# Optimization experiments

Hardware: AMD Instinct MI355X
Metric: run time of the kernel (lower is better)

The kernel has to match this reference:

```python
import math
import jax, jax.numpy as jnp
import numpy as np

B, C, H, W = 2, 512, 64, 64
NUM_HEADS = 8
NUM_GROUPS = 32
EPS = 1e-05
RESCALE = 1.0


def setup_inputs() -> dict:
    key = jax.random.key(0)
    k1, k2, k3 = jax.random.split(key, 3)
    x = jax.random.normal(k1, (B, C, H, W), dtype=jnp.float32)
    norm_w = jnp.ones((C,), dtype=jnp.float32)
    norm_b = jnp.zeros((C,), dtype=jnp.float32)
    qkv_w = jax.random.normal(k2, (3 * C, C), dtype=jnp.float32) * (1.0 / math.sqrt(C))
    qkv_b = jnp.zeros((3 * C,), dtype=jnp.float32)
    proj_w = jax.random.normal(k3, (C, C), dtype=jnp.float32) * (1.0 / math.sqrt(C))
    proj_b = jnp.zeros((C,), dtype=jnp.float32)
    return {"x": x, "norm_w": norm_w, "norm_b": norm_b,
            "qkv_w": qkv_w, "qkv_b": qkv_b, "proj_w": proj_w, "proj_b": proj_b}


def group_norm(x, gamma, beta, num_groups, eps):
    # x: [b, c, h, w]
    b, c = x.shape[0], x.shape[1]
    xg = x.reshape(b, num_groups, -1)  # [b, G, (c//G)*h*w]
    mean = jnp.mean(xg, axis=-1, keepdims=True)
    var = jnp.var(xg, axis=-1, keepdims=True)
    xg = (xg - mean) * jax.lax.rsqrt(var + eps)
    x = xg.reshape(x.shape)
    return x * gamma[None, :, None, None] + beta[None, :, None, None]


def reference(x, norm_w, norm_b, qkv_w, qkv_b, proj_w, proj_b):
    b, c, h, w = x.shape
    L = h * w
    n_heads = NUM_HEADS
    ch = c // n_heads  # per-head channels

    hid = group_norm(x, norm_w, norm_b, NUM_GROUPS, EPS).reshape(b, c, L)
    # 1x1 conv1d == channel matmul
    qkv = jnp.einsum('oc,bcl->bol', qkv_w, hid) + qkv_b[None, :, None]  # [b, 3c, L]
    qkv = qkv.reshape(b * n_heads, 3 * ch, L)
    q, k, v = qkv[:, :ch], qkv[:, ch:2 * ch], qkv[:, 2 * ch:]

    scale = 1.0 / math.sqrt(math.sqrt(ch))
    weight = jnp.einsum('bct,bcs->bts', q * scale, k * scale)  # [b*H, L, L]
    weight = jax.nn.softmax(weight.astype(jnp.float32), axis=-1).astype(weight.dtype)
    a = jnp.einsum('bts,bcs->bct', weight, v)  # [b*H, ch, L]

    hout = a.reshape(b, c, L)
    hout = jnp.einsum('oc,bcl->bol', proj_w, hout) + proj_b[None, :, None]
    hout = hout.reshape(b, c, h, w)
    return (x + hout) / RESCALE
```

## Files before the change

### kernel.cpp

```cpp
#include <hip/hip_runtime.h>
#include <hip/hip_bf16.h>


typedef __attribute__((ext_vector_type(8))) short bf16x8;
typedef __attribute__((ext_vector_type(4))) float f32x4;

#define LL 4096
#define CC 512

__device__ __forceinline__ ushort f2bf(float f) {
    union { float f; unsigned u; } v; v.f = f;
    unsigned u = v.u;
    u += 0x7fffu + ((u >> 16) & 1u);
    return (ushort)(u >> 16);
}

__device__ __forceinline__ float bfly_max16(float x) {
    int a = __float_as_int(x), b = a;
    asm("v_permlane16_swap_b32 %0, %1" : "+v"(a), "+v"(b));
    return fmaxf(__int_as_float(a), __int_as_float(b));
}
__device__ __forceinline__ float bfly_max32(float x) {
    int a = __float_as_int(x), b = a;
    asm("v_permlane32_swap_b32 %0, %1" : "+v"(a), "+v"(b));
    return fmaxf(__int_as_float(a), __int_as_float(b));
}
__device__ __forceinline__ uint cvt_pk_bf16(float lo, float hi) {
    uint r;
    asm("v_cvt_pk_bf16_f32 %0, %1, %2" : "=v"(r) : "v"(lo), "v"(hi));
    return r;
}

__global__ __launch_bounds__(256) void k_convert(
        const float* __restrict__ qkv_w, const float* __restrict__ proj_w,
        ushort* __restrict__ wq, ushort* __restrict__ wp) {
    const int NQ = 1536 * 512;
    int base = (blockIdx.x * 256 + threadIdx.x) * 4;
    const float* src; ushort* dst; int off;
    if (base < NQ) { src = qkv_w; dst = wq; off = base; }
    else           { src = proj_w; dst = wp; off = base - NQ; }
    float4 v = *reinterpret_cast<const float4*>(src + off);
    ushort4 o;
    o.x = f2bf(v.x); o.y = f2bf(v.y); o.z = f2bf(v.z); o.w = f2bf(v.w);
    *reinterpret_cast<ushort4*>(dst + off) = o;
}

__global__ __launch_bounds__(256) void k_gn_part(
        const float* __restrict__ x, float2* __restrict__ part) {
    int bg = blockIdx.x, sl = blockIdx.y;
    const float4* xg = reinterpret_cast<const float4*>(x + (size_t)bg * 65536) + sl * 2048;
    float s = 0.f, ss = 0.f;
    for (int i = threadIdx.x; i < 2048; i += 256) {
        float4 v = xg[i];
        s  += v.x + v.y + v.z + v.w;
        ss += v.x*v.x + v.y*v.y + v.z*v.z + v.w*v.w;
    }
    #pragma unroll
    for (int m = 32; m; m >>= 1) { s += __shfl_xor(s, m); ss += __shfl_xor(ss, m); }
    __shared__ float red[8];
    int wid = threadIdx.x >> 6;
    if ((threadIdx.x & 63) == 0) { red[wid*2] = s; red[wid*2+1] = ss; }
    __syncthreads();
    if (threadIdx.x == 0) {
        s  = red[0] + red[2] + red[4] + red[6];
        ss = red[1] + red[3] + red[5] + red[7];
        part[bg * 8 + sl] = make_float2(s, ss);
    }
}

__global__ void k_gn_stats(const float2* __restrict__ part, float2* __restrict__ stats) {
    int i = threadIdx.x;
    float s = 0.f, ss = 0.f;
    #pragma unroll
    for (int j = 0; j < 8; ++j) { float2 p = part[i*8 + j]; s += p.x; ss += p.y; }
    float mean = s * (1.f/65536.f);
    float var  = ss * (1.f/65536.f) - mean*mean;
    stats[i] = make_float2(mean, rsqrtf(var + 1e-5f));
}

__global__ __launch_bounds__(256) void k_gn_apply(
        const float* __restrict__ x, const float* __restrict__ gamma,
        const float* __restrict__ beta, const float2* __restrict__ stats,
        ushort* __restrict__ hid) {
    int bg = blockIdx.y;
    int b = bg >> 5, c0 = (bg & 31) * 16;
    int l0 = blockIdx.x * 256;
    float2 st = stats[bg];
    __shared__ __align__(16) ushort tile[16][256];
    int tid = threadIdx.x;
    const float* xg = x + (size_t)(b * CC + c0) * LL;
    #pragma unroll
    for (int sub = 0; sub < 4; ++sub) {
        int r = sub * 4 + (tid >> 6);
        int c4 = (tid & 63) * 4;
        float4 v = *reinterpret_cast<const float4*>(xg + (size_t)r * LL + l0 + c4);
        float ga = gamma[c0 + r] * st.y;
        float be = beta[c0 + r] - st.x * ga;
        tile[r][c4+0] = f2bf(v.x * ga + be);
        tile[r][c4+1] = f2bf(v.y * ga + be);
        tile[r][c4+2] = f2bf(v.z * ga + be);
        tile[r][c4+3] = f2bf(v.w * ga + be);
    }
    __syncthreads();
    union { ushort u[16]; uint4 q[2]; } pk;
    #pragma unroll
    for (int r = 0; r < 16; ++r) pk.u[r] = tile[r][tid];
    ushort* dst = hid + ((size_t)b * LL + l0 + tid) * CC + c0;
    *reinterpret_cast<uint4*>(dst)     = pk.q[0];
    *reinterpret_cast<uint4*>(dst + 8) = pk.q[1];
}

#define QSCALE 0.18033688011112042f
__global__ __launch_bounds__(256) void k_qkv(
        const ushort* __restrict__ wq, const ushort* __restrict__ hid,
        const float* __restrict__ qkv_b,
        ushort* __restrict__ q_ws, ushort* __restrict__ k_ws, ushort* __restrict__ v_ws) {
    int b = blockIdx.z;
    int n0 = blockIdx.x * 128;
    int m0 = blockIdx.y * 128;
    int tid = threadIdx.x;
    int w = tid >> 6, lane = tid & 63, h = lane >> 4, lm = lane & 15;
    int m0w = (w & 1) * 64, n0w = (w >> 1) * 64;
    __shared__ __align__(16) ushort As[128][40];
    __shared__ __align__(16) ushort Bs[128][40];
    f32x4 acc[4][4] = {};
    const ushort* Ag = wq + (size_t)m0 * CC;
    const ushort* Bg = hid + (size_t)(b * LL + n0) * CC;
    for (int k0 = 0; k0 < CC; k0 += 32) {
        __syncthreads();
        #pragma unroll
        for (int i = 0; i < 2; ++i) {
            int flat = tid + i * 256;
            int row = flat >> 2, ch = (flat & 3) * 8;
            *reinterpret_cast<uint4*>(&As[row][ch]) =
                *reinterpret_cast<const uint4*>(Ag + (size_t)row * CC + k0 + ch);
            *reinterpret_cast<uint4*>(&Bs[row][ch]) =
                *reinterpret_cast<const uint4*>(Bg + (size_t)row * CC + k0 + ch);
        }
        __syncthreads();
        bf16x8 af[4], bfr[4];
        #pragma unroll
        for (int mi = 0; mi < 4; ++mi)
            af[mi] = *reinterpret_cast<const bf16x8*>(&As[m0w + mi*16 + lm][h*8]);
        #pragma unroll
        for (int nj = 0; nj < 4; ++nj)
            bfr[nj] = *reinterpret_cast<const bf16x8*>(&Bs[n0w + nj*16 + lm][h*8]);
        #pragma unroll
        for (int mi = 0; mi < 4; ++mi)
            #pragma unroll
            for (int nj = 0; nj < 4; ++nj)
                acc[mi][nj] = __builtin_amdgcn_mfma_f32_16x16x32_bf16(af[mi], bfr[nj], acc[mi][nj], 0, 0, 0);
    }
    #pragma unroll
    for (int mi = 0; mi < 4; ++mi) {
        int o_base = m0 + m0w + mi * 16 + h * 4;
        float4 bias = *reinterpret_cast<const float4*>(qkv_b + o_base);
        int head = o_base / 192;
        int rem  = o_base - head * 192;
        int part = rem >> 6;
        int ch   = rem & 63;
        #pragma unroll
        for (int nj = 0; nj < 4; ++nj) {
            int l = n0 + n0w + nj * 16 + lm;
            float v0 = acc[mi][nj][0] + bias.x;
            float v1 = acc[mi][nj][1] + bias.y;
            float v2 = acc[mi][nj][2] + bias.z;
            float v3 = acc[mi][nj][3] + bias.w;
            if (part == 0) {
                ushort4 pk;
                pk.x = f2bf(v0 * QSCALE); pk.y = f2bf(v1 * QSCALE);
                pk.z = f2bf(v2 * QSCALE); pk.w = f2bf(v3 * QSCALE);
                *reinterpret_cast<ushort4*>(q_ws + ((size_t)(b*8 + head) * LL + l) * 64 + ch) = pk;
            } else if (part == 1) {
                ushort4 pk;
                pk.x = f2bf(v0); pk.y = f2bf(v1); pk.z = f2bf(v2); pk.w = f2bf(v3);
                *reinterpret_cast<ushort4*>(k_ws + ((size_t)(b*8 + head) * LL + l) * 64 + ch) = pk;
            } else {
                ushort* vp = v_ws + ((size_t)(b*8 + head) * 64 + ch) * LL + l;
                vp[0] = f2bf(v0); vp[LL] = f2bf(v1); vp[2*LL] = f2bf(v2); vp[3*LL] = f2bf(v3);
            }
        }
    }
}

__global__ __launch_bounds__(256) void k_attn(
        const ushort* __restrict__ q_ws, const ushort* __restrict__ k_ws,
        const ushort* __restrict__ v_ws, ushort* __restrict__ o_ws) {
    int bh = blockIdx.y;
    int tid = threadIdx.x;
    int w = tid >> 6, lane = tid & 63, h = lane >> 4, lm = lane & 15;
    int t0 = blockIdx.x * 128 + w * 32;

    __shared__ __align__(16) ushort Ks [2][64][72];
    __shared__ __align__(16) ushort Vts[2][64][72];

    bf16x8 bQ[2][2];
    {
        const ushort* qp = q_ws + ((size_t)bh * LL + t0 + lm) * 64 + h * 8;
        bQ[0][0] = *reinterpret_cast<const bf16x8*>(qp);
        bQ[0][1] = *reinterpret_cast<const bf16x8*>(qp + 32);
        bQ[1][0] = *reinterpret_cast<const bf16x8*>(qp + 16 * 64);
        bQ[1][1] = *reinterpret_cast<const bf16x8*>(qp + 16 * 64 + 32);
    }
    bf16x8 aOnes;
    {
        short v = (lm == 0) ? (short)0x3F80 : (short)0;
        #pragma unroll
        for (int j = 0; j < 8; ++j) aOnes[j] = v;
    }

    int srow = lane >> 3, scol = (lane & 7) * 8;
    const ushort* kgp = k_ws + ((size_t)bh * LL + w * 16 + srow) * 64 + scol;
    const ushort* vgp = v_ws + ((size_t)bh * 64 + w * 16 + srow) * LL + scol;
    uint4 kr0, kr1, vr0, vr1;
    auto issue = [&]() {
        kr0 = *reinterpret_cast<const uint4*>(kgp);
        kr1 = *reinterpret_cast<const uint4*>(kgp + 8 * 64);
        vr0 = *reinterpret_cast<const uint4*>(vgp);
        vr1 = *reinterpret_cast<const uint4*>(vgp + 8 * LL);
        kgp += 64 * 64;
        vgp += 64;
    };
    issue();

    float mr[2] = {-1e30f, -1e30f};
    f32x4 accO[2][5] = {};

    for (int t = 0; t < 64; ++t) {
        int p = t & 1;
        {
            int row = w * 16 + srow;
            *reinterpret_cast<uint4*>(&Ks [p][row    ][scol]) = kr0;
            *reinterpret_cast<uint4*>(&Ks [p][row + 8][scol]) = kr1;
            *reinterpret_cast<uint4*>(&Vts[p][row    ][scol]) = vr0;
            *reinterpret_cast<uint4*>(&Vts[p][row + 8][scol]) = vr1;
        }
        if (t < 63) issue();
        __syncthreads();

        f32x4 sf[2][4] = {};
        __builtin_amdgcn_s_setprio(1);
        #pragma unroll
        for (int ss = 0; ss < 4; ++ss)
            #pragma unroll
            for (int kc = 0; kc < 2; ++kc) {
                bf16x8 aK = *reinterpret_cast<const bf16x8*>(&Ks[p][ss*16 + lm][kc*32 + h*8]);
                sf[0][ss] = __builtin_amdgcn_mfma_f32_16x16x32_bf16(aK, bQ[0][kc], sf[0][ss], 0, 0, 0);
                sf[1][ss] = __builtin_amdgcn_mfma_f32_16x16x32_bf16(aK, bQ[1][kc], sf[1][ss], 0, 0, 0);
            }
        __builtin_amdgcn_s_setprio(0);

        #pragma unroll
        for (int qt = 0; qt < 2; ++qt) {
            float a0 = fmaxf(fmaxf(sf[qt][0][0], sf[qt][0][1]), fmaxf(sf[qt][0][2], sf[qt][0][3]));
            float a1 = fmaxf(fmaxf(sf[qt][1][0], sf[qt][1][1]), fmaxf(sf[qt][1][2], sf[qt][1][3]));
            float a2 = fmaxf(fmaxf(sf[qt][2][0], sf[qt][2][1]), fmaxf(sf[qt][2][2], sf[qt][2][3]));
            float a3 = fmaxf(fmaxf(sf[qt][3][0], sf[qt][3][1]), fmaxf(sf[qt][3][2], sf[qt][3][3]));
            float tm = fmaxf(fmaxf(a0, a1), fmaxf(a2, a3));
            tm = bfly_max16(tm);
            tm = bfly_max32(tm);
            if (!__all(tm <= mr[qt] + 8.f)) {
                float mn = fmaxf(mr[qt], tm);
                float corr = __builtin_amdgcn_exp2f(mr[qt] - mn);
                mr[qt] = mn;
                #pragma unroll
                for (int nj = 0; nj < 5; ++nj)
                    #pragma unroll
                    for (int r = 0; r < 4; ++r)
                        accO[qt][nj][r] *= corr;
            }
            #pragma unroll
            for (int ss = 0; ss < 4; ++ss)
                #pragma unroll
                for (int r = 0; r < 4; ++r)
                    sf[qt][ss][r] = __builtin_amdgcn_exp2f(sf[qt][ss][r] - mr[qt]);

            bf16x8 bP[2];
            #pragma unroll
            for (int kc = 0; kc < 2; ++kc) {
                uint a = cvt_pk_bf16(sf[qt][2*kc  ][0], sf[qt][2*kc  ][1]);
                uint b = cvt_pk_bf16(sf[qt][2*kc  ][2], sf[qt][2*kc  ][3]);
                uint c = cvt_pk_bf16(sf[qt][2*kc+1][0], sf[qt][2*kc+1][1]);
                uint d = cvt_pk_bf16(sf[qt][2*kc+1][2], sf[qt][2*kc+1][3]);
                asm("v_permlane32_swap_b32 %0, %1" : "+v"(a), "+v"(c));
                asm("v_permlane32_swap_b32 %0, %1" : "+v"(b), "+v"(d));
                asm("v_permlane16_swap_b32 %0, %1" : "+v"(a), "+v"(c));
                asm("v_permlane16_swap_b32 %0, %1" : "+v"(b), "+v"(d));
                union { uint u[4]; bf16x8 v; } pw;
                pw.u[0] = a; pw.u[1] = b; pw.u[2] = c; pw.u[3] = d;
                bP[kc] = pw.v;
            }

            __builtin_amdgcn_s_setprio(1);
            #pragma unroll
            for (int kc = 0; kc < 2; ++kc) {
                #pragma unroll
                for (int nj = 0; nj < 4; ++nj) {
                    bf16x8 aV = *reinterpret_cast<const bf16x8*>(&Vts[p][nj*16 + lm][kc*32 + h*8]);
                    accO[qt][nj] = __builtin_amdgcn_mfma_f32_16x16x32_bf16(aV, bP[kc], accO[qt][nj], 0, 0, 0);
                }
                accO[qt][4] = __builtin_amdgcn_mfma_f32_16x16x32_bf16(aOnes, bP[kc], accO[qt][4], 0, 0, 0);
            }
            __builtin_amdgcn_s_setprio(0);
        }
    }

    #pragma unroll
    for (int qt = 0; qt < 2; ++qt) {
        float l  = __shfl(accO[qt][4][0], lm);
        float iv = 1.f / l;
        #pragma unroll
        for (int nj = 0; nj < 4; ++nj) {
            ushort4 o4;
            o4.x = f2bf(accO[qt][nj][0] * iv);
            o4.y = f2bf(accO[qt][nj][1] * iv);
            o4.z = f2bf(accO[qt][nj][2] * iv);
            o4.w = f2bf(accO[qt][nj][3] * iv);
            *reinterpret_cast<ushort4*>(
                o_ws + ((size_t)bh * LL + t0 + qt*16 + lm) * 64 + nj*16 + h*4) = o4;
        }
    }
}

__global__ __launch_bounds__(256) void k_proj(
        const ushort* __restrict__ wp, const ushort* __restrict__ o_ws,
        const float* __restrict__ proj_b, const float* __restrict__ x,
        float* __restrict__ out) {
    int b = blockIdx.z;
    int n0 = blockIdx.x * 128;
    int m0 = blockIdx.y * 128;
    int tid = threadIdx.x;
    int w = tid >> 6, lane = tid & 63, h = lane >> 4, lm = lane & 15;
    int m0w = (w & 1) * 64, n0w = (w >> 1) * 64;
    __shared__ __align__(16) ushort As[128][40];
    __shared__ __align__(16) ushort Bs[128][40];
    f32x4 acc[4][4] = {};
    const ushort* Ag = wp + (size_t)m0 * CC;
    for (int k0 = 0; k0 < CC; k0 += 32) {
        const ushort* Bg = o_ws + ((size_t)(b * 8 + (k0 >> 6)) * LL + n0) * 64 + (k0 & 63);
        __syncthreads();
        #pragma unroll
        for (int i = 0; i < 2; ++i) {
            int flat = tid + i * 256;
            int row = flat >> 2, ch = (flat & 3) * 8;
            *reinterpret_cast<uint4*>(&As[row][ch]) =
                *reinterpret_cast<const uint4*>(Ag + (size_t)row * CC + k0 + ch);
            *reinterpret_cast<uint4*>(&Bs[row][ch]) =
                *reinterpret_cast<const uint4*>(Bg + (size_t)row * 64 + ch);
        }
        __syncthreads();
        bf16x8 af[4], bfr[4];
        #pragma unroll
        for (int mi = 0; mi < 4; ++mi)
            af[mi] = *reinterpret_cast<const bf16x8*>(&As[m0w + mi*16 + lm][h*8]);
        #pragma unroll
        for (int nj = 0; nj < 4; ++nj)
            bfr[nj] = *reinterpret_cast<const bf16x8*>(&Bs[n0w + nj*16 + lm][h*8]);
        #pragma unroll
        for (int mi = 0; mi < 4; ++mi)
            #pragma unroll
            for (int nj = 0; nj < 4; ++nj)
                acc[mi][nj] = __builtin_amdgcn_mfma_f32_16x16x32_bf16(af[mi], bfr[nj], acc[mi][nj], 0, 0, 0);
    }
    #pragma unroll
    for (int mi = 0; mi < 4; ++mi) {
        int o = m0 + m0w + mi * 16 + h * 4;
        float4 bias = *reinterpret_cast<const float4*>(proj_b + o);
        #pragma unroll
        for (int nj = 0; nj < 4; ++nj) {
            int l = n0 + n0w + nj * 16 + lm;
            size_t xo = (size_t)(b * CC + o) * LL + l;
            out[xo]          = acc[mi][nj][0] + bias.x + x[xo];
            out[xo +   LL]   = acc[mi][nj][1] + bias.y + x[xo +   LL];
            out[xo + 2*LL]   = acc[mi][nj][2] + bias.z + x[xo + 2*LL];
            out[xo + 3*LL]   = acc[mi][nj][3] + bias.w + x[xo + 3*LL];
        }
    }
}

extern "C" void kernel_launch(void* const* d_in, const int* in_sizes, int n_in,
                              void* d_out, int out_size, void* d_ws, size_t ws_size,
                              hipStream_t stream) {
    const float* x      = (const float*)d_in[0];
    const float* norm_w = (const float*)d_in[1];
    const float* norm_b = (const float*)d_in[2];
    const float* qkv_w  = (const float*)d_in[3];
    const float* qkv_b  = (const float*)d_in[4];
    const float* proj_w = (const float*)d_in[5];
    const float* proj_b = (const float*)d_in[6];
    float* out = (float*)d_out;
    char* ws = (char*)d_ws;

    ushort* wq    = (ushort*)(ws);
    ushort* wp    = (ushort*)(ws + 1572864);
    ushort* hid   = (ushort*)(ws + 2097152);
    ushort* q_ws  = (ushort*)(ws + 10485760);
    ushort* k_ws  = (ushort*)(ws + 18874368);
    ushort* v_ws  = (ushort*)(ws + 27262976);
    ushort* o_ws  = (ushort*)(ws + 35651584);
    float2* part  = (float2*)(ws + 44040192);
    float2* stats = (float2*)(ws + 44044288);

    k_convert<<<dim3(1024), dim3(256), 0, stream>>>(qkv_w, proj_w, wq, wp);
    k_gn_part<<<dim3(64, 8), dim3(256), 0, stream>>>(x, part);
    k_gn_stats<<<dim3(1), dim3(64), 0, stream>>>(part, stats);
    k_gn_apply<<<dim3(16, 64), dim3(256), 0, stream>>>(x, norm_w, norm_b, stats, hid);
    k_qkv<<<dim3(32, 12, 2), dim3(256), 0, stream>>>(wq, hid, qkv_b, q_ws, k_ws, v_ws);
    k_attn<<<dim3(32, 16), dim3(256), 0, stream>>>(q_ws, k_ws, v_ws, o_ws);
    k_proj<<<dim3(32, 4, 2), dim3(256), 0, stream>>>(wp, o_ws, proj_b, x, out);
}
```

Baseline: 174.0 us.

## Split attention KV range across two warp groups and switch to fp16

Every bf16 intermediate and MFMA is switched to fp16. The attention kernel now launches 512 threads, and two groups of four waves each process half of the key/value sequence. The groups merge their partial softmax states (max, sum, accumulator) through shared memory at the end. The ones-vector MFMA that computed the row sum is replaced by explicit lane reductions. The aim is more waves per block and fewer serial KV iterations per wave, paid for with a merge step, more shared memory, fp16 range risk, and removal of the lazy-rescale threshold, so rescaling happens more often.

```diff
diff --git a/kernel.cpp b/kernel.cpp
--- a/kernel.cpp
+++ b/kernel.cpp
@@ -2,17 +2,16 @@
 #include <hip/hip_bf16.h>
 
 
-typedef __attribute__((ext_vector_type(8))) short bf16x8;
+typedef _Float16 f16;
+typedef __attribute__((ext_vector_type(8))) _Float16 f16x8;
 typedef __attribute__((ext_vector_type(4))) float f32x4;
 
 #define LL 4096
 #define CC 512
 
-__device__ __forceinline__ ushort f2bf(float f) {
-    union { float f; unsigned u; } v; v.f = f;
-    unsigned u = v.u;
-    u += 0x7fffu + ((u >> 16) & 1u);
-    return (ushort)(u >> 16);
+__device__ __forceinline__ ushort f2h(float f) {
+    f16 h = (f16)f;
+    return *reinterpret_cast<ushort*>(&h);
 }
 
 __device__ __forceinline__ float bfly_max16(float x) {
@@ -25,10 +24,20 @@
     asm("v_permlane32_swap_b32 %0, %1" : "+v"(a), "+v"(b));
     return fmaxf(__int_as_float(a), __int_as_float(b));
 }
-__device__ __forceinline__ uint cvt_pk_bf16(float lo, float hi) {
-    uint r;
-    asm("v_cvt_pk_bf16_f32 %0, %1, %2" : "=v"(r) : "v"(lo), "v"(hi));
-    return r;
+__device__ __forceinline__ float bfly_add16(float x) {
+    int a = __float_as_int(x), b = a;
+    asm("v_permlane16_swap_b32 %0, %1" : "+v"(a), "+v"(b));
+    return __int_as_float(a) + __int_as_float(b);
+}
+__device__ __forceinline__ float bfly_add32(float x) {
+    int a = __float_as_int(x), b = a;
+    asm("v_permlane32_swap_b32 %0, %1" : "+v"(a), "+v"(b));
+    return __int_as_float(a) + __int_as_float(b);
+}
+__device__ __forceinline__ uint pkh(float lo, float hi) {
+    union { decltype(__builtin_amdgcn_cvt_pkrtz(0.f, 0.f)) h; uint u; } r;
+    r.h = __builtin_amdgcn_cvt_pkrtz(lo, hi);
+    return r.u;
 }
 
 __global__ __launch_bounds__(256) void k_convert(
@@ -41,7 +50,7 @@
     else           { src = proj_w; dst = wp; off = base - NQ; }
     float4 v = *reinterpret_cast<const float4*>(src + off);
     ushort4 o;
-    o.x = f2bf(v.x); o.y = f2bf(v.y); o.z = f2bf(v.z); o.w = f2bf(v.w);
+    o.x = f2h(v.x); o.y = f2h(v.y); o.z = f2h(v.z); o.w = f2h(v.w);
     *reinterpret_cast<ushort4*>(dst + off) = o;
 }
 
@@ -96,10 +105,10 @@
         float4 v = *reinterpret_cast<const float4*>(xg + (size_t)r * LL + l0 + c4);
         float ga = gamma[c0 + r] * st.y;
         float be = beta[c0 + r] - st.x * ga;
-        tile[r][c4+0] = f2bf(v.x * ga + be);
-        tile[r][c4+1] = f2bf(v.y * ga + be);
-        tile[r][c4+2] = f2bf(v.z * ga + be);
-        tile[r][c4+3] = f2bf(v.w * ga + be);
+        tile[r][c4+0] = f2h(v.x * ga + be);
+        tile[r][c4+1] = f2h(v.y * ga + be);
+        tile[r][c4+2] = f2h(v.z * ga + be);
+        tile[r][c4+3] = f2h(v.w * ga + be);
     }
     __syncthreads();
     union { ushort u[16]; uint4 q[2]; } pk;
@@ -138,18 +147,18 @@
                 *reinterpret_cast<const uint4*>(Bg + (size_t)row * CC + k0 + ch);
         }
         __syncthreads();
-        bf16x8 af[4], bfr[4];
+        f16x8 af[4], bfr[4];
         #pragma unroll
         for (int mi = 0; mi < 4; ++mi)
-            af[mi] = *reinterpret_cast<const bf16x8*>(&As[m0w + mi*16 + lm][h*8]);
+            af[mi] = *reinterpret_cast<const f16x8*>(&As[m0w + mi*16 + lm][h*8]);
         #pragma unroll
         for (int nj = 0; nj < 4; ++nj)
-            bfr[nj] = *reinterpret_cast<const bf16x8*>(&Bs[n0w + nj*16 + lm][h*8]);
+            bfr[nj] = *reinterpret_cast<const f16x8*>(&Bs[n0w + nj*16 + lm][h*8]);
         #pragma unroll
         for (int mi = 0; mi < 4; ++mi)
             #pragma unroll
             for (int nj = 0; nj < 4; ++nj)
-                acc[mi][nj] = __builtin_amdgcn_mfma_f32_16x16x32_bf16(af[mi], bfr[nj], acc[mi][nj], 0, 0, 0);
+                acc[mi][nj] = __builtin_amdgcn_mfma_f32_16x16x32_f16(af[mi], bfr[nj], acc[mi][nj], 0, 0, 0);
     }
     #pragma unroll
     for (int mi = 0; mi < 4; ++mi) {
@@ -168,50 +177,47 @@
             float v3 = acc[mi][nj][3] + bias.w;
             if (part == 0) {
                 ushort4 pk;
-                pk.x = f2bf(v0 * QSCALE); pk.y = f2bf(v1 * QSCALE);
-                pk.z = f2bf(v2 * QSCALE); pk.w = f2bf(v3 * QSCALE);
+                pk.x = f2h(v0 * QSCALE); pk.y = f2h(v1 * QSCALE);
+                pk.z = f2h(v2 * QSCALE); pk.w = f2h(v3 * QSCALE);
                 *reinterpret_cast<ushort4*>(q_ws + ((size_t)(b*8 + head) * LL + l) * 64 + ch) = pk;
             } else if (part == 1) {
                 ushort4 pk;
-                pk.x = f2bf(v0); pk.y = f2bf(v1); pk.z = f2bf(v2); pk.w = f2bf(v3);
+                pk.x = f2h(v0); pk.y = f2h(v1); pk.z = f2h(v2); pk.w = f2h(v3);
                 *reinterpret_cast<ushort4*>(k_ws + ((size_t)(b*8 + head) * LL + l) * 64 + ch) = pk;
             } else {
                 ushort* vp = v_ws + ((size_t)(b*8 + head) * 64 + ch) * LL + l;
-                vp[0] = f2bf(v0); vp[LL] = f2bf(v1); vp[2*LL] = f2bf(v2); vp[3*LL] = f2bf(v3);
+                vp[0] = f2h(v0); vp[LL] = f2h(v1); vp[2*LL] = f2h(v2); vp[3*LL] = f2h(v3);
             }
         }
     }
 }
 
-__global__ __launch_bounds__(256) void k_attn(
+__global__ __launch_bounds__(512, 4) void k_attn(
         const ushort* __restrict__ q_ws, const ushort* __restrict__ k_ws,
         const ushort* __restrict__ v_ws, ushort* __restrict__ o_ws) {
     int bh = blockIdx.y;
     int tid = threadIdx.x;
     int w = tid >> 6, lane = tid & 63, h = lane >> 4, lm = lane & 15;
-    int t0 = blockIdx.x * 128 + w * 32;
-
-    __shared__ __align__(16) ushort Ks [2][64][72];
-    __shared__ __align__(16) ushort Vts[2][64][72];
-
-    bf16x8 bQ[2][2];
+    int g = w >> 2, w4 = w & 3;
+    int t0 = blockIdx.x * 128 + w4 * 32;
+
+    __shared__ __align__(16) char smem[2 * 36864];
+    ushort (*Ks)[2][64][72]  = reinterpret_cast<ushort(*)[2][64][72]>(smem);
+    ushort (*Vts)[2][64][72] = reinterpret_cast<ushort(*)[2][64][72]>(smem + 36864);
+    float* msc = reinterpret_cast<float*>(smem);
+
+    f16x8 bQ[2][2];
     {
         const ushort* qp = q_ws + ((size_t)bh * LL + t0 + lm) * 64 + h * 8;
-        bQ[0][0] = *reinterpret_cast<const bf16x8*>(qp);
-        bQ[0][1] = *reinterpret_cast<const bf16x8*>(qp + 32);
-        bQ[1][0] = *reinterpret_cast<const bf16x8*>(qp + 16 * 64);
-        bQ[1][1] = *reinterpret_cast<const bf16x8*>(qp + 16 * 64 + 32);
-    }
-    bf16x8 aOnes;
-    {
-        short v = (lm == 0) ? (short)0x3F80 : (short)0;
-        #pragma unroll
-        for (int j = 0; j < 8; ++j) aOnes[j] = v;
+        bQ[0][0] = *reinterpret_cast<const f16x8*>(qp);
+        bQ[0][1] = *reinterpret_cast<const f16x8*>(qp + 32);
+        bQ[1][0] = *reinterpret_cast<const f16x8*>(qp + 16 * 64);
+        bQ[1][1] = *reinterpret_cast<const f16x8*>(qp + 16 * 64 + 32);
     }
 
     int srow = lane >> 3, scol = (lane & 7) * 8;
-    const ushort* kgp = k_ws + ((size_t)bh * LL + w * 16 + srow) * 64 + scol;
-    const ushort* vgp = v_ws + ((size_t)bh * 64 + w * 16 + srow) * LL + scol;
+    const ushort* kgp = k_ws + ((size_t)bh * LL + g * 2048 + w4 * 16 + srow) * 64 + scol;
+    const ushort* vgp = v_ws + ((size_t)bh * 64 + w4 * 16 + srow) * LL + g * 2048 + scol;
     uint4 kr0, kr1, vr0, vr1;
     auto issue = [&]() {
         kr0 = *reinterpret_cast<const uint4*>(kgp);
@@ -224,18 +230,19 @@
     issue();
 
     float mr[2] = {-1e30f, -1e30f};
-    f32x4 accO[2][5] = {};
-
-    for (int t = 0; t < 64; ++t) {
+    float lr[2] = {0.f, 0.f};
+    f32x4 accO[2][4] = {};
+
+    for (int t = 0; t < 32; ++t) {
         int p = t & 1;
         {
-            int row = w * 16 + srow;
-            *reinterpret_cast<uint4*>(&Ks [p][row    ][scol]) = kr0;
-            *reinterpret_cast<uint4*>(&Ks [p][row + 8][scol]) = kr1;
-            *reinterpret_cast<uint4*>(&Vts[p][row    ][scol]) = vr0;
-            *reinterpret_cast<uint4*>(&Vts[p][row + 8][scol]) = vr1;
-        }
-        if (t < 63) issue();
+            int row = w4 * 16 + srow;
+            *reinterpret_cast<uint4*>(&Ks [g][p][row    ][scol]) = kr0;
+            *reinterpret_cast<uint4*>(&Ks [g][p][row + 8][scol]) = kr1;
+            *reinterpret_cast<uint4*>(&Vts[g][p][row    ][scol]) = vr0;
+            *reinterpret_cast<uint4*>(&Vts[g][p][row + 8][scol]) = vr1;
+        }
+        if (t < 31) issue();
         __syncthreads();
 
         f32x4 sf[2][4] = {};
@@ -244,9 +251,9 @@
         for (int ss = 0; ss < 4; ++ss)
             #pragma unroll
             for (int kc = 0; kc < 2; ++kc) {
-                bf16x8 aK = *reinterpret_cast<const bf16x8*>(&Ks[p][ss*16 + lm][kc*32 + h*8]);
-                sf[0][ss] = __builtin_amdgcn_mfma_f32_16x16x32_bf16(aK, bQ[0][kc], sf[0][ss], 0, 0, 0);
-                sf[1][ss] = __builtin_amdgcn_mfma_f32_16x16x32_bf16(aK, bQ[1][kc], sf[1][ss], 0, 0, 0);
+                f16x8 aK = *reinterpret_cast<const f16x8*>(&Ks[g][p][ss*16 + lm][kc*32 + h*8]);
+                sf[0][ss] = __builtin_amdgcn_mfma_f32_16x16x32_f16(aK, bQ[0][kc], sf[0][ss], 0, 0, 0);
+                sf[1][ss] = __builtin_amdgcn_mfma_f32_16x16x32_f16(aK, bQ[1][kc], sf[1][ss], 0, 0, 0);
             }
         __builtin_amdgcn_s_setprio(0);
 
@@ -259,12 +266,13 @@
             float tm = fmaxf(fmaxf(a0, a1), fmaxf(a2, a3));
             tm = bfly_max16(tm);
             tm = bfly_max32(tm);
-            if (!__all(tm <= mr[qt] + 8.f)) {
+            if (!__all(tm <= mr[qt])) {
                 float mn = fmaxf(mr[qt], tm);
                 float corr = __builtin_amdgcn_exp2f(mr[qt] - mn);
                 mr[qt] = mn;
+                lr[qt] *= corr;
                 #pragma unroll
-                for (int nj = 0; nj < 5; ++nj)
+                for (int nj = 0; nj < 4; ++nj)
                     #pragma unroll
                     for (int r = 0; r < 4; ++r)
                         accO[qt][nj][r] *= corr;
@@ -275,49 +283,76 @@
                 for (int r = 0; r < 4; ++r)
                     sf[qt][ss][r] = __builtin_amdgcn_exp2f(sf[qt][ss][r] - mr[qt]);
 
-            bf16x8 bP[2];
+            float rs = (((sf[qt][0][0] + sf[qt][0][1]) + (sf[qt][0][2] + sf[qt][0][3]))
+                      + ((sf[qt][1][0] + sf[qt][1][1]) + (sf[qt][1][2] + sf[qt][1][3])))
+                     + (((sf[qt][2][0] + sf[qt][2][1]) + (sf[qt][2][2] + sf[qt][2][3]))
+                      + ((sf[qt][3][0] + sf[qt][3][1]) + (sf[qt][3][2] + sf[qt][3][3])));
+            rs = bfly_add16(rs);
+            rs = bfly_add32(rs);
+            lr[qt] += rs;
+
+            f16x8 bP[2];
             #pragma unroll
             for (int kc = 0; kc < 2; ++kc) {
-                uint a = cvt_pk_bf16(sf[qt][2*kc  ][0], sf[qt][2*kc  ][1]);
-                uint b = cvt_pk_bf16(sf[qt][2*kc  ][2], sf[qt][2*kc  ][3]);
-                uint c = cvt_pk_bf16(sf[qt][2*kc+1][0], sf[qt][2*kc+1][1]);
-                uint d = cvt_pk_bf16(sf[qt][2*kc+1][2], sf[qt][2*kc+1][3]);
+                uint a = pkh(sf[qt][2*kc  ][0], sf[qt][2*kc  ][1]);
+                uint b = pkh(sf[qt][2*kc  ][2], sf[qt][2*kc  ][3]);
+                uint c = pkh(sf[qt][2*kc+1][0], sf[qt][2*kc+1][1]);
+                uint d = pkh(sf[qt][2*kc+1][2], sf[qt][2*kc+1][3]);
                 asm("v_permlane32_swap_b32 %0, %1" : "+v"(a), "+v"(c));
                 asm("v_permlane32_swap_b32 %0, %1" : "+v"(b), "+v"(d));
                 asm("v_permlane16_swap_b32 %0, %1" : "+v"(a), "+v"(c));
                 asm("v_permlane16_swap_b32 %0, %1" : "+v"(b), "+v"(d));
-                union { uint u[4]; bf16x8 v; } pw;
+                union { uint u[4]; f16x8 v; } pw;
                 pw.u[0] = a; pw.u[1] = b; pw.u[2] = c; pw.u[3] = d;
                 bP[kc] = pw.v;
             }
 
             __builtin_amdgcn_s_setprio(1);
             #pragma unroll
-            for (int kc = 0; kc < 2; ++kc) {
+            for (int kc = 0; kc < 2; ++kc)
                 #pragma unroll
                 for (int nj = 0; nj < 4; ++nj) {
-                    bf16x8 aV = *reinterpret_cast<const bf16x8*>(&Vts[p][nj*16 + lm][kc*32 + h*8]);
-                    accO[qt][nj] = __builtin_amdgcn_mfma_f32_16x16x32_bf16(aV, bP[kc], accO[qt][nj], 0, 0, 0);
+                    f16x8 aV = *reinterpret_cast<const f16x8*>(&Vts[g][p][nj*16 + lm][kc*32 + h*8]);
+                    accO[qt][nj] = __builtin_amdgcn_mfma_f32_16x16x32_f16(aV, bP[kc], accO[qt][nj], 0, 0, 0);
                 }
-                accO[qt][4] = __builtin_amdgcn_mfma_f32_16x16x32_bf16(aOnes, bP[kc], accO[qt][4], 0, 0, 0);
+            __builtin_amdgcn_s_setprio(0);
+        }
+    }
+
+    __syncthreads();
+    if (g == 1) {
+        float* dst = msc + (size_t)(w4 * 64 + lane) * 36;
+        #pragma unroll
+        for (int qt = 0; qt < 2; ++qt)
+            #pragma unroll
+            for (int nj = 0; nj < 4; ++nj)
+                #pragma unroll
+                for (int r = 0; r < 4; ++r)
+                    dst[(qt * 4 + nj) * 4 + r] = accO[qt][nj][r];
+        dst[32] = lr[0]; dst[33] = lr[1];
+        dst[34] = mr[0]; dst[35] = mr[1];
+    }
+    __syncthreads();
+    if (g == 0) {
+        const float* src = msc + (size_t)(w4 * 64 + lane) * 36;
+        #pragma unroll
+        for (int qt = 0; qt < 2; ++qt) {
+            float m1 = src[34 + qt];
+            float M  = fmaxf(mr[qt], m1);
+            float c0 = __builtin_amdgcn_exp2f(mr[qt] - M);
+            float c1 = __builtin_amdgcn_exp2f(m1 - M);
+            float l  = lr[qt] * c0 + src[32 + qt] * c1;
+            float iv = 1.f / l;
+            #pragma unroll
+            for (int nj = 0; nj < 4; ++nj) {
+                ushort4 o4;
+                o4.x = f2h((accO[qt][nj][0] * c0 + src[(qt*4+nj)*4 + 0] * c1) * iv);
+                o4.y = f2h((accO[qt][nj][1] * c0 + src[(qt*4+nj)*4 + 1] * c1) * iv);
+                o4.z = f2h((accO[qt][nj][2] * c0 + src[(qt*4+nj)*4 + 2] * c1) * iv);
+                o4.w = f2h((accO[qt][nj][3] * c0 + src[(qt*4+nj)*4 + 3] * c1) * iv);
+                *reinterpret_cast<ushort4*>(
+                    o_ws + ((size_t)bh * LL + t0 + qt*16 + lm) * 64 + nj*16 + h*4) = o4;
             }
-            __builtin_amdgcn_s_setprio(0);
-        }
-    }
-
-    #pragma unroll
-    for (int qt = 0; qt < 2; ++qt) {
-        float l  = __shfl(accO[qt][4][0], lm);
-        float iv = 1.f / l;
-        #pragma unroll
-        for (int nj = 0; nj < 4; ++nj) {
-            ushort4 o4;
-            o4.x = f2bf(accO[qt][nj][0] * iv);
-            o4.y = f2bf(accO[qt][nj][1] * iv);
-            o4.z = f2bf(accO[qt][nj][2] * iv);
-            o4.w = f2bf(accO[qt][nj][3] * iv);
-            *reinterpret_cast<ushort4*>(
-                o_ws + ((size_t)bh * LL + t0 + qt*16 + lm) * 64 + nj*16 + h*4) = o4;
         }
     }
 }
@@ -349,18 +384,18 @@
                 *reinterpret_cast<const uint4*>(Bg + (size_t)row * 64 + ch);
         }
         __syncthreads();
-        bf16x8 af[4], bfr[4];
+        f16x8 af[4], bfr[4];
         #pragma unroll
         for (int mi = 0; mi < 4; ++mi)
-            af[mi] = *reinterpret_cast<const bf16x8*>(&As[m0w + mi*16 + lm][h*8]);
+            af[mi] = *reinterpret_cast<const f16x8*>(&As[m0w + mi*16 + lm][h*8]);
         #pragma unroll
         for (int nj = 0; nj < 4; ++nj)
-            bfr[nj] = *reinterpret_cast<const bf16x8*>(&Bs[n0w + nj*16 + lm][h*8]);
+            bfr[nj] = *reinterpret_cast<const f16x8*>(&Bs[n0w + nj*16 + lm][h*8]);
         #pragma unroll
         for (int mi = 0; mi < 4; ++mi)
             #pragma unroll
             for (int nj = 0; nj < 4; ++nj)
-                acc[mi][nj] = __builtin_amdgcn_mfma_f32_16x16x32_bf16(af[mi], bfr[nj], acc[mi][nj], 0, 0, 0);
+                acc[mi][nj] = __builtin_amdgcn_mfma_f32_16x16x32_f16(af[mi], bfr[nj], acc[mi][nj], 0, 0, 0);
     }
     #pragma unroll
     for (int mi = 0; mi < 4; ++mi) {
@@ -406,6 +441,6 @@
     k_gn_stats<<<dim3(1), dim3(64), 0, stream>>>(part, stats);
     k_gn_apply<<<dim3(16, 64), dim3(256), 0, stream>>>(x, norm_w, norm_b, stats, hid);
     k_qkv<<<dim3(32, 12, 2), dim3(256), 0, stream>>>(wq, hid, qkv_b, q_ws, k_ws, v_ws);
-    k_attn<<<dim3(32, 16), dim3(256), 0, stream>>>(q_ws, k_ws, v_ws, o_ws);
+    k_attn<<<dim3(32, 16), dim3(512), 0, stream>>>(q_ws, k_ws, v_ws, o_ws);
     k_proj<<<dim3(32, 4, 2), dim3(256), 0, stream>>>(wp, o_ws, proj_b, x, out);
 }
```

Result: slower. 178.4 us (+2.5%).
